# Kernel optimization log

Hardware: AMD Instinct MI355X
Metric: run time of the kernel (lower is better)

## Reference

```python
import jax, jax.numpy as jnp
import numpy as np

B, S, D_MODEL = 2, 2048, 2048
N_HEADS, D_HEAD = 32, 64
SEQ_MAX = 2048


def _rope_cache(seq_len, d_head):
    half = d_head // 2
    inv_freq = 1.0 / (10000.0 ** (np.arange(0, half, dtype=np.float32) / half))
    t = np.arange(seq_len, dtype=np.float32)
    freqs = np.einsum('i,j->ij', t, inv_freq)  # [S, half]
    emb = np.concatenate([freqs, freqs], axis=-1)  # [S, d_head]
    return jnp.asarray(np.cos(emb)), jnp.asarray(np.sin(emb))


def _rotate_half(x):
    half = x.shape[-1] // 2
    return jnp.concatenate([-x[..., half:], x[..., :half]], axis=-1)


def setup_inputs() -> dict:
    key = jax.random.key(0)
    ks = jax.random.split(key, 9)
    std = 0.02
    mk = lambda k: jax.random.normal(k, (D_MODEL, D_MODEL), jnp.float32) * std
    return {
        'x': jax.random.normal(ks[0], (B, S, D_MODEL), jnp.float32),
        'Wq': mk(ks[1]), 'bq': jnp.zeros((D_MODEL,), jnp.float32),
        'Wk': mk(ks[2]), 'bk': jnp.zeros((D_MODEL,), jnp.float32),
        'Wv': mk(ks[3]), 'bv': jnp.zeros((D_MODEL,), jnp.float32),
        'Wo': mk(ks[4]), 'bo': jnp.zeros((D_MODEL,), jnp.float32),
    }


def reference(x, Wq, bq, Wk, bk, Wv, bv, Wo, bo):
    Bsz, S_len, _ = x.shape
    # projections (torch Linear: y = x @ W^T + b)
    q = x @ Wq.T + bq
    k = x @ Wk.T + bk
    v = x @ Wv.T + bv
    # [B, H, S, Dh]
    to_heads = lambda t: t.reshape(Bsz, S_len, N_HEADS, D_HEAD).transpose(0, 2, 1, 3)
    q, k, v = to_heads(q), to_heads(k), to_heads(v)
    cos, sin = _rope_cache(S_len, D_HEAD)  # [S, Dh]
    cos = cos[None, None]
    sin = sin[None, None]
    q = q * cos + _rotate_half(q) * sin
    k = k * cos + _rotate_half(k) * sin
    scale = 1.0 / jnp.sqrt(jnp.float32(D_HEAD))
    att = jnp.einsum('bhqd,bhkd->bhqk', q, k) * scale
    causal = jnp.tril(jnp.ones((S_len, S_len), dtype=bool))
    att = jnp.where(causal[None, None], att, jnp.float32(-jnp.inf))
    att = jax.nn.softmax(att, axis=-1)
    # sigmoid-gated values (dropout = identity at inference)
    y = jnp.einsum('bhqk,bhkd->bhqd', att, jax.nn.sigmoid(v))
    y = y.transpose(0, 2, 1, 3).reshape(Bsz, S_len, D_MODEL)
    return y @ Wo.T + bo
```

## Files before the change

kernel.cpp:

```cpp
#include <hip/hip_runtime.h>

typedef unsigned short u16;
typedef float f32x4 __attribute__((ext_vector_type(4)));
typedef __bf16 bf16x8 __attribute__((ext_vector_type(8)));

#define S_LEN 2048
#define DM 2048
#define NHEAD 32
#define DHEAD 64

__device__ __forceinline__ u16 f2bf(float f) {
    __bf16 b = (__bf16)f;
    return __builtin_bit_cast(u16, b);
}
__device__ __forceinline__ void async16(const void* g, void* l) {
    __builtin_amdgcn_global_load_lds(
        (const __attribute__((address_space(1))) unsigned int*)g,
        (__attribute__((address_space(3))) unsigned int*)l, 16, 0, 0);
}
__device__ __forceinline__ void fast_sincos(float th, float* s, float* c) {
    float rev = th * 0.15915494309189535f;
    rev = rev - floorf(rev);
    *s = __builtin_amdgcn_sinf(rev);
    *c = __builtin_amdgcn_cosf(rev);
}
__device__ __forceinline__ float fexp2(float x) { return __builtin_amdgcn_exp2f(x); }

__global__ __launch_bounds__(256) void cast_all(const float* __restrict__ x,
                                                const float* __restrict__ Wq,
                                                const float* __restrict__ Wk,
                                                const float* __restrict__ Wv,
                                                const float* __restrict__ Wo,
                                                u16* __restrict__ xb,
                                                u16* __restrict__ Wqkv,
                                                u16* __restrict__ Wob) {
    int bid = blockIdx.x;
    const float* src;
    u16* dst;
    long long off;
    if (bid < 8192)       { src = x;  dst = xb;             off = (long long)bid * 1024; }
    else if (bid < 12288) { src = Wq; dst = Wqkv;           off = (long long)(bid - 8192) * 1024; }
    else if (bid < 16384) { src = Wk; dst = Wqkv + 4194304; off = (long long)(bid - 12288) * 1024; }
    else if (bid < 20480) { src = Wv; dst = Wqkv + 8388608; off = (long long)(bid - 16384) * 1024; }
    else                  { src = Wo; dst = Wob;            off = (long long)(bid - 20480) * 1024; }
    long long i = off + threadIdx.x * 4;
    float4 f = *(const float4*)(src + i);
    ushort4 v;
    v.x = f2bf(f.x); v.y = f2bf(f.y); v.z = f2bf(f.z); v.w = f2bf(f.w);
    *(ushort4*)(dst + i) = v;
}

__global__ __launch_bounds__(256) void gemm_qkv(const u16* __restrict__ A,
                                                const u16* __restrict__ Bt,
                                                const float* __restrict__ bq,
                                                const float* __restrict__ bk,
                                                const float* __restrict__ bv,
                                                u16* __restrict__ Qo, u16* __restrict__ Ko,
                                                u16* __restrict__ VTo, int M, int K) {
    __shared__ __align__(16) u16 As[128 * 32];
    __shared__ __align__(16) u16 Bs[128 * 32];
    int tid = threadIdx.x;
    int w = tid >> 6, lane = tid & 63, quad = lane >> 4, l16 = lane & 15;
    int m0 = blockIdx.x * 128;
    int n0 = blockIdx.y * 128;
    int sel = n0 >> 11;
    int nloc = n0 & 2047;
    int wm = (w & 1) * 64, wn = (w >> 1) * 64;

    f32x4 acc[4][4] = {};
    const u16* ga = A + (long long)m0 * K;
    const u16* gb = Bt + (long long)n0 * K;

    for (int k0 = 0; k0 < K; k0 += 32) {
#pragma unroll
        for (int rr = 0; rr < 2; ++rr) {
            int c = tid + rr * 256;
            int row = c >> 2, kc = c & 3;
            async16(ga + (long long)row * K + k0 + kc * 8, (char*)As + c * 16);
            async16(gb + (long long)row * K + k0 + kc * 8, (char*)Bs + c * 16);
        }
        __syncthreads();
        bf16x8 af[4], bfv[4];
#pragma unroll
        for (int mt = 0; mt < 4; ++mt)
            af[mt] = *(const bf16x8*)(As + (wm + mt * 16 + l16) * 32 + quad * 8);
#pragma unroll
        for (int nt = 0; nt < 4; ++nt)
            bfv[nt] = *(const bf16x8*)(Bs + (wn + nt * 16 + l16) * 32 + quad * 8);
#pragma unroll
        for (int mt = 0; mt < 4; ++mt)
#pragma unroll
            for (int nt = 0; nt < 4; ++nt)
                acc[mt][nt] = __builtin_amdgcn_mfma_f32_16x16x32_bf16(af[mt], bfv[nt],
                                                                      acc[mt][nt], 0, 0, 0);
        __syncthreads();
    }

    if (sel < 2) {
        float scale = sel == 0 ? 0.18033688011112042f : 1.0f;
        u16* out = sel == 0 ? Qo : Ko;
        const float* bias = sel == 0 ? bq : bk;
#pragma unroll
        for (int ntl = 0; ntl < 2; ++ntl) {
            int col = nloc + wn + ntl * 16 + l16;
            int j = (ntl * 16 + l16) & 31;
            float inv = __expf(-(float)j * 0.28782313662425575f);
            float ci, si;
            fast_sincos(inv, &si, &ci);
            float b1 = bias[col], b2 = bias[col + 32];
#pragma unroll
            for (int mt = 0; mt < 4; ++mt) {
                int rowb = m0 + wm + mt * 16 + quad * 4;
                int s0 = rowb & (S_LEN - 1);
                float sn, cs;
                fast_sincos((float)s0 * inv, &sn, &cs);
#pragma unroll
                for (int r = 0; r < 4; ++r) {
                    int row = rowb + r;
                    float x1 = acc[mt][ntl][r] + b1;
                    float x2 = acc[mt][ntl + 2][r] + b2;
                    out[(long long)row * 2048 + col] = f2bf((x1 * cs - x2 * sn) * scale);
                    out[(long long)row * 2048 + col + 32] = f2bf((x2 * cs + x1 * sn) * scale);
                    float c2 = cs * ci - sn * si;
                    float s2 = sn * ci + cs * si;
                    cs = c2; sn = s2;
                }
            }
        }
    } else {
#pragma unroll
        for (int mt = 0; mt < 4; ++mt) {
            int rowb = m0 + wm + mt * 16 + quad * 4;
            int b = rowb >> 11;
            int s0 = rowb & (S_LEN - 1);
#pragma unroll
            for (int nt = 0; nt < 4; ++nt) {
                int col = nloc + wn + nt * 16 + l16;
                int h = col >> 6, d = col & 63;
                float bvs = bv[col];
                ushort4 pk;
                pk.x = f2bf(1.f / (1.f + __expf(-(acc[mt][nt][0] + bvs))));
                pk.y = f2bf(1.f / (1.f + __expf(-(acc[mt][nt][1] + bvs))));
                pk.z = f2bf(1.f / (1.f + __expf(-(acc[mt][nt][2] + bvs))));
                pk.w = f2bf(1.f / (1.f + __expf(-(acc[mt][nt][3] + bvs))));
                *(ushort4*)(VTo + ((long long)((b * NHEAD + h) * DHEAD + d)) * S_LEN + s0) = pk;
            }
        }
    }
}

__global__ __launch_bounds__(256) void gemm_bt_f32(const u16* __restrict__ A,
                                                   const u16* __restrict__ Bt,
                                                   const float* __restrict__ bias,
                                                   float* __restrict__ Cout,
                                                   int M, int N, int K) {
    __shared__ __align__(16) u16 As[128 * 32];
    __shared__ __align__(16) u16 Bs[128 * 32];
    int tid = threadIdx.x;
    int w = tid >> 6, lane = tid & 63, quad = lane >> 4, l16 = lane & 15;
    int m0 = blockIdx.x * 128;
    int n0 = blockIdx.y * 128;
    int wm = (w & 1) * 64, wn = (w >> 1) * 64;

    f32x4 acc[4][4] = {};
    const u16* ga = A + (long long)m0 * K;
    const u16* gb = Bt + (long long)n0 * K;

    for (int k0 = 0; k0 < K; k0 += 32) {
#pragma unroll
        for (int rr = 0; rr < 2; ++rr) {
            int c = tid + rr * 256;
            int row = c >> 2, kc = c & 3;
            async16(ga + (long long)row * K + k0 + kc * 8, (char*)As + c * 16);
            async16(gb + (long long)row * K + k0 + kc * 8, (char*)Bs + c * 16);
        }
        __syncthreads();
        bf16x8 af[4], bfv[4];
#pragma unroll
        for (int mt = 0; mt < 4; ++mt)
            af[mt] = *(const bf16x8*)(As + (wm + mt * 16 + l16) * 32 + quad * 8);
#pragma unroll
        for (int nt = 0; nt < 4; ++nt)
            bfv[nt] = *(const bf16x8*)(Bs + (wn + nt * 16 + l16) * 32 + quad * 8);
#pragma unroll
        for (int mt = 0; mt < 4; ++mt)
#pragma unroll
            for (int nt = 0; nt < 4; ++nt)
                acc[mt][nt] = __builtin_amdgcn_mfma_f32_16x16x32_bf16(af[mt], bfv[nt],
                                                                      acc[mt][nt], 0, 0, 0);
        __syncthreads();
    }

#pragma unroll
    for (int mt = 0; mt < 4; ++mt) {
#pragma unroll
        for (int nt = 0; nt < 4; ++nt) {
            int col = n0 + wn + nt * 16 + l16;
            float bvs = bias[col];
#pragma unroll
            for (int r = 0; r < 4; ++r) {
                int row = m0 + wm + mt * 16 + quad * 4 + r;
                Cout[(long long)row * N + col] = acc[mt][nt][r] + bvs;
            }
        }
    }
}

__global__ __launch_bounds__(256, 4) void flash_attn(const u16* __restrict__ Q,
                                                     const u16* __restrict__ K,
                                                     const u16* __restrict__ VT,
                                                     u16* __restrict__ Y) {
    int bid = blockIdx.x;
    int pi = bid & 15;
    int h = (bid >> 4) & 31;
    int b = bid >> 9;
    int tid = threadIdx.x;
    int w = tid >> 6, lane = tid & 63, quad = lane >> 4, l16 = lane & 15;

    __shared__ __align__(16) u16 Kl[2][64 * 64];
    __shared__ __align__(16) u16 Vl[2][64 * 64];
    __shared__ __align__(16) u16 Pl[4][16 * 64];

    const u16* kbase = K + ((long long)(b * S_LEN)) * DM + h * DHEAD;
    const u16* vbase = VT + ((long long)((b * NHEAD + h) * DHEAD)) * S_LEN;

    bf16x8 kpre[2], vpre[2];
    int c0 = tid, c1 = tid + 256;
    int row0 = c0 >> 3, lc0 = (c0 & 7) ^ (row0 & 7);
    int row1 = c1 >> 3, lc1 = (c1 & 7) ^ (row1 & 7);

    kpre[0] = *(const bf16x8*)(kbase + (long long)row0 * DM + lc0 * 8);
    vpre[0] = *(const bf16x8*)(vbase + (long long)row0 * S_LEN + lc0 * 8);
    kpre[1] = *(const bf16x8*)(kbase + (long long)row1 * DM + lc1 * 8);
    vpre[1] = *(const bf16x8*)(vbase + (long long)row1 * S_LEN + lc1 * 8);

    int it = 0;
#pragma unroll 1
    for (int rep = 0; rep < 2; ++rep) {
        int qt = rep ? 31 - pi : pi;
        int qrow = qt * 64 + w * 16 + l16;
        const u16* qp = Q + ((long long)(b * S_LEN + qrow)) * DM + h * DHEAD + quad * 8;
        bf16x8 aq0 = *(const bf16x8*)(qp);
        bf16x8 aq1 = *(const bf16x8*)(qp + 32);

        f32x4 o[4] = {};
        float m_r = -__builtin_inff(), l_r = 0.f;

#pragma unroll 1
        for (int kt = 0; kt <= qt; ++kt) {
            int k0 = kt * 64;
            u16* Kb_ = Kl[it & 1];
            u16* Vb_ = Vl[it & 1];
            *(bf16x8*)((char*)Kb_ + c0 * 16) = kpre[0];
            *(bf16x8*)((char*)Vb_ + c0 * 16) = vpre[0];
            *(bf16x8*)((char*)Kb_ + c1 * 16) = kpre[1];
            *(bf16x8*)((char*)Vb_ + c1 * 16) = vpre[1];
            {
                int nk0 = (kt < qt ? kt + 1 : 0) * 64;
                kpre[0] = *(const bf16x8*)(kbase + (long long)(nk0 + row0) * DM + lc0 * 8);
                vpre[0] = *(const bf16x8*)(vbase + (long long)row0 * S_LEN + nk0 + lc0 * 8);
                kpre[1] = *(const bf16x8*)(kbase + (long long)(nk0 + row1) * DM + lc1 * 8);
                vpre[1] = *(const bf16x8*)(vbase + (long long)row1 * S_LEN + nk0 + lc1 * 8);
            }
            __syncthreads();

            f32x4 s[4];
#pragma unroll
            for (int nt = 0; nt < 4; ++nt) {
                int row = nt * 16 + l16;
                int sw0 = (quad ^ (row & 7)) * 8;
                int sw1 = ((quad + 4) ^ (row & 7)) * 8;
                bf16x8 ak0 = *(const bf16x8*)(Kb_ + row * 64 + sw0);
                bf16x8 ak1 = *(const bf16x8*)(Kb_ + row * 64 + sw1);
                f32x4 a = {};
                a = __builtin_amdgcn_mfma_f32_16x16x32_bf16(ak0, aq0, a, 0, 0, 0);
                a = __builtin_amdgcn_mfma_f32_16x16x32_bf16(ak1, aq1, a, 0, 0, 0);
                s[nt] = a;
            }
            if (kt == qt) {
                int qg = qt * 64 + w * 16 + l16;
#pragma unroll
                for (int nt = 0; nt < 4; ++nt) {
#pragma unroll
                    for (int r = 0; r < 4; ++r) {
                        int kc = k0 + nt * 16 + quad * 4 + r;
                        if (kc > qg) s[nt][r] = -__builtin_inff();
                    }
                }
            }
            float mx = s[0][0];
#pragma unroll
            for (int nt = 0; nt < 4; ++nt)
#pragma unroll
                for (int r = 0; r < 4; ++r) mx = fmaxf(mx, s[nt][r]);
            mx = fmaxf(mx, __shfl_xor(mx, 16, 64));
            mx = fmaxf(mx, __shfl_xor(mx, 32, 64));
            float mnew = fmaxf(m_r, mx);
            float alpha = fexp2(m_r - mnew);
            m_r = mnew;
#pragma unroll
            for (int nt = 0; nt < 4; ++nt)
#pragma unroll
                for (int r = 0; r < 4; ++r) s[nt][r] = fexp2(s[nt][r] - mnew);
            float sum = 0.f;
#pragma unroll
            for (int nt = 0; nt < 4; ++nt)
#pragma unroll
                for (int r = 0; r < 4; ++r) sum += s[nt][r];
            sum += __shfl_xor(sum, 16, 64);
            sum += __shfl_xor(sum, 32, 64);
            l_r = l_r * alpha + sum;

#pragma unroll
            for (int dt = 0; dt < 4; ++dt)
#pragma unroll
                for (int r = 0; r < 4; ++r) o[dt][r] *= alpha;

            u16* pw = &Pl[w][0];
#pragma unroll
            for (int nt = 0; nt < 4; ++nt) {
                ushort4 pk;
                pk.x = f2bf(s[nt][0]); pk.y = f2bf(s[nt][1]);
                pk.z = f2bf(s[nt][2]); pk.w = f2bf(s[nt][3]);
                int chunk = (nt * 2 + (quad >> 1)) ^ (l16 & 7);
                *(ushort4*)(pw + l16 * 64 + chunk * 8 + (quad & 1) * 4) = pk;
            }
            bf16x8 bp0 = *(const bf16x8*)(pw + l16 * 64 + (quad ^ (l16 & 7)) * 8);
            bf16x8 bp1 = *(const bf16x8*)(pw + l16 * 64 + ((quad + 4) ^ (l16 & 7)) * 8);
#pragma unroll
            for (int dt = 0; dt < 4; ++dt) {
                int row = dt * 16 + l16;
                int sw0 = (quad ^ (row & 7)) * 8;
                int sw1 = ((quad + 4) ^ (row & 7)) * 8;
                bf16x8 av0 = *(const bf16x8*)(Vb_ + row * 64 + sw0);
                bf16x8 av1 = *(const bf16x8*)(Vb_ + row * 64 + sw1);
                o[dt] = __builtin_amdgcn_mfma_f32_16x16x32_bf16(av0, bp0, o[dt], 0, 0, 0);
                o[dt] = __builtin_amdgcn_mfma_f32_16x16x32_bf16(av1, bp1, o[dt], 0, 0, 0);
            }
            ++it;
        }

        float inv_l = 1.f / l_r;
        u16* yp = Y + ((long long)(b * S_LEN + qt * 64 + w * 16 + l16)) * DM + h * DHEAD;
#pragma unroll
        for (int dt = 0; dt < 4; ++dt) {
            ushort4 yk;
            yk.x = f2bf(o[dt][0] * inv_l);
            yk.y = f2bf(o[dt][1] * inv_l);
            yk.z = f2bf(o[dt][2] * inv_l);
            yk.w = f2bf(o[dt][3] * inv_l);
            *(ushort4*)(yp + dt * 16 + quad * 4) = yk;
        }
    }
}

extern "C" void kernel_launch(void* const* d_in, const int* in_sizes, int n_in,
                              void* d_out, int out_size, void* d_ws, size_t ws_size,
                              hipStream_t stream) {
    const float* x  = (const float*)d_in[0];
    const float* Wq = (const float*)d_in[1];
    const float* bq = (const float*)d_in[2];
    const float* Wk = (const float*)d_in[3];
    const float* bk = (const float*)d_in[4];
    const float* Wv = (const float*)d_in[5];
    const float* bv = (const float*)d_in[6];
    const float* Wo = (const float*)d_in[7];
    const float* bo = (const float*)d_in[8];

    const long long M = 2LL * S_LEN;

    char* ws = (char*)d_ws;
    u16* xb   = (u16*)(ws);
    u16* Wqkv = (u16*)(ws + 16 * 1024 * 1024);
    u16* Wob  = (u16*)(ws + 40 * 1024 * 1024);
    u16* Qb   = (u16*)(ws + 48 * 1024 * 1024);
    u16* Kb   = (u16*)(ws + 64 * 1024 * 1024);
    u16* VTb  = (u16*)(ws + 80 * 1024 * 1024);
    u16* Yb   = (u16*)(ws + 96 * 1024 * 1024);

    cast_all<<<24576, 256, 0, stream>>>(x, Wq, Wk, Wv, Wo, xb, Wqkv, Wob);

    dim3 gqkv(32, 48);
    gemm_qkv<<<gqkv, 256, 0, stream>>>(xb, Wqkv, bq, bk, bv, Qb, Kb, VTb, (int)M, DM);

    flash_attn<<<2 * NHEAD * 16, 256, 0, stream>>>(Qb, Kb, VTb, Yb);

    dim3 gg(32, 16);
    gemm_bt_f32<<<gg, 256, 0, stream>>>(Yb, Wob, bo, (float*)d_out, (int)M, DM, DM);
}
```

Baseline: 452.9 us.

## Enlarge attention query tile to 128 rows and split RoPE into separate kernel

Each flash attention block now processes 128 query rows, with two 16-row sub-tiles per wave. Each K/V tile loaded into LDS is therefore reused across twice as many queries, and the grid is halved. RoPE rotation and Q scaling move out of the QKV GEMM epilogue into a standalone rope_qk kernel that reads and rewrites Q and K in place. This simplifies the GEMM epilogue, but it adds a full extra pass over Q and K in global memory and lowers flash attention occupancy (launch bounds drop from 4 to 2).

```diff
diff --git a/kernel.cpp b/kernel.cpp
--- a/kernel.cpp
+++ b/kernel.cpp
@@ -12,6 +12,9 @@
 __device__ __forceinline__ u16 f2bf(float f) {
     __bf16 b = (__bf16)f;
     return __builtin_bit_cast(u16, b);
+}
+__device__ __forceinline__ float bf2f(u16 u) {
+    return (float)__builtin_bit_cast(__bf16, u);
 }
 __device__ __forceinline__ void async16(const void* g, void* l) {
     __builtin_amdgcn_global_load_lds(
@@ -50,6 +53,26 @@
     *(ushort4*)(dst + i) = v;
 }
 
+__global__ __launch_bounds__(256) void rope_qk(u16* __restrict__ Qb, u16* __restrict__ Kb) {
+    long long idx = (long long)blockIdx.x * 256 + threadIdx.x;
+    int which = (int)(idx >> 22);
+    int t = (int)(idx & 4194303);
+    int j = t & 31;
+    int h = (t >> 5) & 31;
+    int row = t >> 10;
+    int s = row & (S_LEN - 1);
+    u16* T = which ? Kb : Qb;
+    float scale = which ? 1.0f : 0.18033688011112042f;
+    long long base = (long long)row * DM + h * DHEAD;
+    float inv = __expf(-(float)j * 0.28782313662425575f);
+    float sn, cs;
+    fast_sincos((float)s * inv, &sn, &cs);
+    float x1 = bf2f(T[base + j]);
+    float x2 = bf2f(T[base + 32 + j]);
+    T[base + j] = f2bf((x1 * cs - x2 * sn) * scale);
+    T[base + 32 + j] = f2bf((x2 * cs + x1 * sn) * scale);
+}
+
 __global__ __launch_bounds__(256) void gemm_qkv(const u16* __restrict__ A,
                                                 const u16* __restrict__ Bt,
                                                 const float* __restrict__ bq,
@@ -97,33 +120,18 @@
     }
 
     if (sel < 2) {
-        float scale = sel == 0 ? 0.18033688011112042f : 1.0f;
         u16* out = sel == 0 ? Qo : Ko;
         const float* bias = sel == 0 ? bq : bk;
 #pragma unroll
-        for (int ntl = 0; ntl < 2; ++ntl) {
-            int col = nloc + wn + ntl * 16 + l16;
-            int j = (ntl * 16 + l16) & 31;
-            float inv = __expf(-(float)j * 0.28782313662425575f);
-            float ci, si;
-            fast_sincos(inv, &si, &ci);
-            float b1 = bias[col], b2 = bias[col + 32];
-#pragma unroll
-            for (int mt = 0; mt < 4; ++mt) {
-                int rowb = m0 + wm + mt * 16 + quad * 4;
-                int s0 = rowb & (S_LEN - 1);
-                float sn, cs;
-                fast_sincos((float)s0 * inv, &sn, &cs);
+        for (int mt = 0; mt < 4; ++mt) {
+#pragma unroll
+            for (int nt = 0; nt < 4; ++nt) {
+                int col = nloc + wn + nt * 16 + l16;
+                float bvs = bias[col];
 #pragma unroll
                 for (int r = 0; r < 4; ++r) {
-                    int row = rowb + r;
-                    float x1 = acc[mt][ntl][r] + b1;
-                    float x2 = acc[mt][ntl + 2][r] + b2;
-                    out[(long long)row * 2048 + col] = f2bf((x1 * cs - x2 * sn) * scale);
-                    out[(long long)row * 2048 + col + 32] = f2bf((x2 * cs + x1 * sn) * scale);
-                    float c2 = cs * ci - sn * si;
-                    float s2 = sn * ci + cs * si;
-                    cs = c2; sn = s2;
+                    int row = m0 + wm + mt * 16 + quad * 4 + r;
+                    out[(long long)row * 2048 + col] = f2bf(acc[mt][nt][r] + bvs);
                 }
             }
         }
@@ -206,20 +214,20 @@
     }
 }
 
-__global__ __launch_bounds__(256, 4) void flash_attn(const u16* __restrict__ Q,
+__global__ __launch_bounds__(256, 2) void flash_attn(const u16* __restrict__ Q,
                                                      const u16* __restrict__ K,
                                                      const u16* __restrict__ VT,
                                                      u16* __restrict__ Y) {
     int bid = blockIdx.x;
-    int pi = bid & 15;
-    int h = (bid >> 4) & 31;
-    int b = bid >> 9;
+    int pi = bid & 7;
+    int h = (bid >> 3) & 31;
+    int b = bid >> 8;
     int tid = threadIdx.x;
     int w = tid >> 6, lane = tid & 63, quad = lane >> 4, l16 = lane & 15;
 
     __shared__ __align__(16) u16 Kl[2][64 * 64];
     __shared__ __align__(16) u16 Vl[2][64 * 64];
-    __shared__ __align__(16) u16 Pl[4][16 * 64];
+    __shared__ __align__(16) u16 Pl[4][32 * 64];
 
     const u16* kbase = K + ((long long)(b * S_LEN)) * DM + h * DHEAD;
     const u16* vbase = VT + ((long long)((b * NHEAD + h) * DHEAD)) * S_LEN;
@@ -237,18 +245,23 @@
     int it = 0;
 #pragma unroll 1
     for (int rep = 0; rep < 2; ++rep) {
-        int qt = rep ? 31 - pi : pi;
-        int qrow = qt * 64 + w * 16 + l16;
-        const u16* qp = Q + ((long long)(b * S_LEN + qrow)) * DM + h * DHEAD + quad * 8;
-        bf16x8 aq0 = *(const bf16x8*)(qp);
-        bf16x8 aq1 = *(const bf16x8*)(qp + 32);
-
-        f32x4 o[4] = {};
-        float m_r = -__builtin_inff(), l_r = 0.f;
-
+        int qt = rep ? 15 - pi : pi;
+        bf16x8 aq[2][2];
+#pragma unroll
+        for (int sub = 0; sub < 2; ++sub) {
+            int qrow = qt * 128 + w * 32 + sub * 16 + l16;
+            const u16* qp = Q + ((long long)(b * S_LEN + qrow)) * DM + h * DHEAD + quad * 8;
+            aq[sub][0] = *(const bf16x8*)(qp);
+            aq[sub][1] = *(const bf16x8*)(qp + 32);
+        }
+
+        f32x4 o[2][4] = {};
+        float m_r[2] = {-__builtin_inff(), -__builtin_inff()};
+        float l_r[2] = {0.f, 0.f};
+
+        int kts = 2 * qt + 2;
 #pragma unroll 1
-        for (int kt = 0; kt <= qt; ++kt) {
-            int k0 = kt * 64;
+        for (int kt = 0; kt < kts; ++kt) {
             u16* Kb_ = Kl[it & 1];
             u16* Vb_ = Vl[it & 1];
             *(bf16x8*)((char*)Kb_ + c0 * 16) = kpre[0];
@@ -256,7 +269,7 @@
             *(bf16x8*)((char*)Kb_ + c1 * 16) = kpre[1];
             *(bf16x8*)((char*)Vb_ + c1 * 16) = vpre[1];
             {
-                int nk0 = (kt < qt ? kt + 1 : 0) * 64;
+                int nk0 = (kt + 1 < kts ? kt + 1 : 0) * 64;
                 kpre[0] = *(const bf16x8*)(kbase + (long long)(nk0 + row0) * DM + lc0 * 8);
                 vpre[0] = *(const bf16x8*)(vbase + (long long)row0 * S_LEN + nk0 + lc0 * 8);
                 kpre[1] = *(const bf16x8*)(kbase + (long long)(nk0 + row1) * DM + lc1 * 8);
@@ -264,92 +277,107 @@
             }
             __syncthreads();
 
-            f32x4 s[4];
+            bf16x8 ak0[4], ak1[4];
 #pragma unroll
             for (int nt = 0; nt < 4; ++nt) {
                 int row = nt * 16 + l16;
-                int sw0 = (quad ^ (row & 7)) * 8;
-                int sw1 = ((quad + 4) ^ (row & 7)) * 8;
-                bf16x8 ak0 = *(const bf16x8*)(Kb_ + row * 64 + sw0);
-                bf16x8 ak1 = *(const bf16x8*)(Kb_ + row * 64 + sw1);
-                f32x4 a = {};
-                a = __builtin_amdgcn_mfma_f32_16x16x32_bf16(ak0, aq0, a, 0, 0, 0);
-                a = __builtin_amdgcn_mfma_f32_16x16x32_bf16(ak1, aq1, a, 0, 0, 0);
-                s[nt] = a;
-            }
-            if (kt == qt) {
-                int qg = qt * 64 + w * 16 + l16;
+                ak0[nt] = *(const bf16x8*)(Kb_ + row * 64 + (quad ^ (row & 7)) * 8);
+                ak1[nt] = *(const bf16x8*)(Kb_ + row * 64 + ((quad + 4) ^ (row & 7)) * 8);
+            }
+
+            bf16x8 bp[2][2];
+            u16* pw = &Pl[w][0];
+#pragma unroll
+            for (int sub = 0; sub < 2; ++sub) {
+                f32x4 s[4];
 #pragma unroll
                 for (int nt = 0; nt < 4; ++nt) {
-#pragma unroll
-                    for (int r = 0; r < 4; ++r) {
-                        int kc = k0 + nt * 16 + quad * 4 + r;
-                        if (kc > qg) s[nt][r] = -__builtin_inff();
+                    f32x4 a = {};
+                    a = __builtin_amdgcn_mfma_f32_16x16x32_bf16(ak0[nt], aq[sub][0], a, 0, 0, 0);
+                    a = __builtin_amdgcn_mfma_f32_16x16x32_bf16(ak1[nt], aq[sub][1], a, 0, 0, 0);
+                    s[nt] = a;
+                }
+                if (kt >= 2 * qt) {
+                    int qg = qt * 128 + w * 32 + sub * 16 + l16;
+#pragma unroll
+                    for (int nt = 0; nt < 4; ++nt) {
+#pragma unroll
+                        for (int r = 0; r < 4; ++r) {
+                            int kg = kt * 64 + nt * 16 + quad * 4 + r;
+                            if (kg > qg) s[nt][r] = -__builtin_inff();
+                        }
                     }
                 }
-            }
-            float mx = s[0][0];
-#pragma unroll
-            for (int nt = 0; nt < 4; ++nt)
-#pragma unroll
-                for (int r = 0; r < 4; ++r) mx = fmaxf(mx, s[nt][r]);
-            mx = fmaxf(mx, __shfl_xor(mx, 16, 64));
-            mx = fmaxf(mx, __shfl_xor(mx, 32, 64));
-            float mnew = fmaxf(m_r, mx);
-            float alpha = fexp2(m_r - mnew);
-            m_r = mnew;
-#pragma unroll
-            for (int nt = 0; nt < 4; ++nt)
-#pragma unroll
-                for (int r = 0; r < 4; ++r) s[nt][r] = fexp2(s[nt][r] - mnew);
-            float sum = 0.f;
-#pragma unroll
-            for (int nt = 0; nt < 4; ++nt)
-#pragma unroll
-                for (int r = 0; r < 4; ++r) sum += s[nt][r];
-            sum += __shfl_xor(sum, 16, 64);
-            sum += __shfl_xor(sum, 32, 64);
-            l_r = l_r * alpha + sum;
-
-#pragma unroll
-            for (int dt = 0; dt < 4; ++dt)
-#pragma unroll
-                for (int r = 0; r < 4; ++r) o[dt][r] *= alpha;
-
-            u16* pw = &Pl[w][0];
-#pragma unroll
-            for (int nt = 0; nt < 4; ++nt) {
-                ushort4 pk;
-                pk.x = f2bf(s[nt][0]); pk.y = f2bf(s[nt][1]);
-                pk.z = f2bf(s[nt][2]); pk.w = f2bf(s[nt][3]);
-                int chunk = (nt * 2 + (quad >> 1)) ^ (l16 & 7);
-                *(ushort4*)(pw + l16 * 64 + chunk * 8 + (quad & 1) * 4) = pk;
-            }
-            bf16x8 bp0 = *(const bf16x8*)(pw + l16 * 64 + (quad ^ (l16 & 7)) * 8);
-            bf16x8 bp1 = *(const bf16x8*)(pw + l16 * 64 + ((quad + 4) ^ (l16 & 7)) * 8);
+                float mx = s[0][0];
+#pragma unroll
+                for (int nt = 0; nt < 4; ++nt)
+#pragma unroll
+                    for (int r = 0; r < 4; ++r) mx = fmaxf(mx, s[nt][r]);
+                mx = fmaxf(mx, __shfl_xor(mx, 16, 64));
+                mx = fmaxf(mx, __shfl_xor(mx, 32, 64));
+                float mnew = fmaxf(m_r[sub], mx);
+                float alpha = fexp2(m_r[sub] - mnew);
+                m_r[sub] = mnew;
+#pragma unroll
+                for (int nt = 0; nt < 4; ++nt)
+#pragma unroll
+                    for (int r = 0; r < 4; ++r) s[nt][r] = fexp2(s[nt][r] - mnew);
+                float sum = 0.f;
+#pragma unroll
+                for (int nt = 0; nt < 4; ++nt)
+#pragma unroll
+                    for (int r = 0; r < 4; ++r) sum += s[nt][r];
+                sum += __shfl_xor(sum, 16, 64);
+                sum += __shfl_xor(sum, 32, 64);
+                l_r[sub] = l_r[sub] * alpha + sum;
+#pragma unroll
+                for (int dt = 0; dt < 4; ++dt)
+#pragma unroll
+                    for (int r = 0; r < 4; ++r) o[sub][dt][r] *= alpha;
+
+                int prow = sub * 16 + l16;
+#pragma unroll
+                for (int nt = 0; nt < 4; ++nt) {
+                    ushort4 pk;
+                    pk.x = f2bf(s[nt][0]); pk.y = f2bf(s[nt][1]);
+                    pk.z = f2bf(s[nt][2]); pk.w = f2bf(s[nt][3]);
+                    int chunk = (nt * 2 + (quad >> 1)) ^ (l16 & 7);
+                    *(ushort4*)(pw + prow * 64 + chunk * 8 + (quad & 1) * 4) = pk;
+                }
+                bp[sub][0] = *(const bf16x8*)(pw + prow * 64 + (quad ^ (l16 & 7)) * 8);
+                bp[sub][1] = *(const bf16x8*)(pw + prow * 64 + ((quad + 4) ^ (l16 & 7)) * 8);
+            }
+
 #pragma unroll
             for (int dt = 0; dt < 4; ++dt) {
                 int row = dt * 16 + l16;
-                int sw0 = (quad ^ (row & 7)) * 8;
-                int sw1 = ((quad + 4) ^ (row & 7)) * 8;
-                bf16x8 av0 = *(const bf16x8*)(Vb_ + row * 64 + sw0);
-                bf16x8 av1 = *(const bf16x8*)(Vb_ + row * 64 + sw1);
-                o[dt] = __builtin_amdgcn_mfma_f32_16x16x32_bf16(av0, bp0, o[dt], 0, 0, 0);
-                o[dt] = __builtin_amdgcn_mfma_f32_16x16x32_bf16(av1, bp1, o[dt], 0, 0, 0);
+                bf16x8 av0 = *(const bf16x8*)(Vb_ + row * 64 + (quad ^ (row & 7)) * 8);
+                bf16x8 av1 = *(const bf16x8*)(Vb_ + row * 64 + ((quad + 4) ^ (row & 7)) * 8);
+#pragma unroll
+                for (int sub = 0; sub < 2; ++sub) {
+                    o[sub][dt] = __builtin_amdgcn_mfma_f32_16x16x32_bf16(av0, bp[sub][0],
+                                                                         o[sub][dt], 0, 0, 0);
+                    o[sub][dt] = __builtin_amdgcn_mfma_f32_16x16x32_bf16(av1, bp[sub][1],
+                                                                         o[sub][dt], 0, 0, 0);
+                }
             }
             ++it;
         }
 
-        float inv_l = 1.f / l_r;
-        u16* yp = Y + ((long long)(b * S_LEN + qt * 64 + w * 16 + l16)) * DM + h * DHEAD;
-#pragma unroll
-        for (int dt = 0; dt < 4; ++dt) {
-            ushort4 yk;
-            yk.x = f2bf(o[dt][0] * inv_l);
-            yk.y = f2bf(o[dt][1] * inv_l);
-            yk.z = f2bf(o[dt][2] * inv_l);
-            yk.w = f2bf(o[dt][3] * inv_l);
-            *(ushort4*)(yp + dt * 16 + quad * 4) = yk;
+#pragma unroll
+        for (int sub = 0; sub < 2; ++sub) {
+            float inv_l = 1.f / l_r[sub];
+            u16* yp = Y + ((long long)(b * S_LEN + qt * 128 + w * 32 + sub * 16 + l16)) * DM
+                      + h * DHEAD;
+#pragma unroll
+            for (int dt = 0; dt < 4; ++dt) {
+                ushort4 yk;
+                yk.x = f2bf(o[sub][dt][0] * inv_l);
+                yk.y = f2bf(o[sub][dt][1] * inv_l);
+                yk.z = f2bf(o[sub][dt][2] * inv_l);
+                yk.w = f2bf(o[sub][dt][3] * inv_l);
+                *(ushort4*)(yp + dt * 16 + quad * 4) = yk;
+            }
         }
     }
 }
@@ -383,7 +411,9 @@
     dim3 gqkv(32, 48);
     gemm_qkv<<<gqkv, 256, 0, stream>>>(xb, Wqkv, bq, bk, bv, Qb, Kb, VTb, (int)M, DM);
 
-    flash_attn<<<2 * NHEAD * 16, 256, 0, stream>>>(Qb, Kb, VTb, Yb);
+    rope_qk<<<32768, 256, 0, stream>>>(Qb, Kb);
+
+    flash_attn<<<2 * NHEAD * 8, 256, 0, stream>>>(Qb, Kb, VTb, Yb);
 
     dim3 gg(32, 16);
     gemm_bt_f32<<<gg, 256, 0, stream>>>(Yb, Wob, bo, (float*)d_out, (int)M, DM, DM);
```

Measured after the change: 431.1 us. 1.05x faster.
